# Optimization experiments

Measured on AMD Instinct MI355X. Metric: run time of the kernel, lower is better.

Reference implementation:

```python
import jax, jax.numpy as jnp
import numpy as np

# ---- static config (matches init_kwargs) ----
WS = 7            # window_size
SHIFT = 3         # shift_size (SW-MSA block)
Z, X, Y = 14, 28, 56
DIM = 384
HEADS = 12
HD = DIM // HEADS
N = WS ** 3       # tokens per 3D window = 343
SCALE = HD ** (-0.5)
TBL = (2 * WS - 1) ** 3
B = 2
L = Z * X * Y
NW = (Z // WS) * (X // WS) * (Y // WS)  # 64 windows
MLP_H = 4 * DIM


def _rel_index():
    # Faithful to source: only coords 0 and 1 are offset, coord 0 scaled by (2*Wx-1).
    c = np.stack(np.meshgrid(np.arange(WS), np.arange(WS), np.arange(WS), indexing='ij')).reshape(3, -1)
    r = (c[:, :, None] - c[:, None, :]).transpose(1, 2, 0).astype(np.int64)
    r[..., 0] += WS - 1
    r[..., 1] += WS - 1
    r[..., 0] *= 2 * WS - 1
    idx = r.sum(-1)
    return np.mod(idx, TBL)  # torch wraps negative indices; mod reproduces that

REL_IDX = jnp.asarray(_rel_index())  # (N, N)


def _attn_mask():
    img = np.zeros((1, Z, X, Y, 1))
    sl = (slice(0, -WS), slice(-WS, -SHIFT), slice(-SHIFT, None))
    cnt = 0
    for a in sl:
        for b in sl:
            for c in sl:
                img[:, a, b, c, :] = cnt
                cnt += 1
    w = img.reshape(1, Z // WS, WS, X // WS, WS, Y // WS, WS, 1)
    w = w.transpose(0, 1, 3, 5, 2, 4, 6, 7).reshape(-1, N)
    d = w[:, None, :] - w[:, :, None]
    return np.where(d != 0, -100.0, 0.0).astype(np.float32)  # (NW, N, N)

ATTN_MASK = jnp.asarray(_attn_mask())


def _ln(x, g, b):
    m = x.mean(-1, keepdims=True)
    v = jnp.mean(jnp.square(x - m), axis=-1, keepdims=True)
    return (x - m) * jax.lax.rsqrt(v + 1e-5) * g + b


def _window_partition(x):  # (B,Z,X,Y,C) -> (B*NW, N, C)
    x = x.reshape(B, Z // WS, WS, X // WS, WS, Y // WS, WS, DIM)
    x = x.transpose(0, 1, 3, 5, 2, 4, 6, 7)
    return x.reshape(-1, N, DIM)


def _window_reverse(w):  # (B*NW, N, C) -> (B,Z,X,Y,C)
    x = w.reshape(B, Z // WS, X // WS, Y // WS, WS, WS, WS, DIM)
    x = x.transpose(0, 1, 4, 2, 5, 3, 6, 7)
    return x.reshape(B, Z, X, Y, DIM)


def setup_inputs() -> dict:
    key = jax.random.key(0)
    ks = jax.random.split(key, 8)
    f32 = jnp.float32
    p = {}
    p['x'] = jax.random.normal(ks[0], (B, L, DIM), f32)
    p['norm1_g'] = jnp.ones((DIM,), f32)
    p['norm1_b'] = jnp.zeros((DIM,), f32)
    p['qkv_w'] = (jax.random.normal(ks[1], (DIM, 3 * DIM), f32) * 0.02)
    p['qkv_b'] = jnp.zeros((3 * DIM,), f32)
    p['proj_w'] = (jax.random.normal(ks[2], (DIM, DIM), f32) * 0.02)
    p['proj_b'] = jnp.zeros((DIM,), f32)
    p['rel_tbl'] = (jax.random.normal(ks[3], (TBL, HEADS), f32) * 0.02)
    p['norm2_g'] = jnp.ones((DIM,), f32)
    p['norm2_b'] = jnp.zeros((DIM,), f32)
    p['fc1_w'] = (jax.random.normal(ks[4], (DIM, MLP_H), f32) * 0.02)
    p['fc1_b'] = jnp.zeros((MLP_H,), f32)
    p['fc2_w'] = (jax.random.normal(ks[5], (MLP_H, DIM), f32) * 0.02)
    p['fc2_b'] = jnp.zeros((DIM,), f32)
    return p


def reference(x, norm1_g, norm1_b, qkv_w, qkv_b, proj_w, proj_b, rel_tbl,
              norm2_g, norm2_b, fc1_w, fc1_b, fc2_w, fc2_b):
    shortcut = x
    h = _ln(x, norm1_g, norm1_b).reshape(B, Z, X, Y, DIM)
    # cyclic shift
    h = jnp.roll(h, (-SHIFT, -SHIFT, -SHIFT), axis=(1, 2, 3))
    w = _window_partition(h)                       # (B*NW, N, C)
    qkv = (w @ qkv_w + qkv_b).reshape(-1, N, 3, HEADS, HD).transpose(2, 0, 3, 1, 4)
    q, k, v = qkv[0] * SCALE, qkv[1], qkv[2]       # (B*NW, H, N, hd)
    attn = jnp.einsum('bhnd,bhmd->bhnm', q, k)
    bias = rel_tbl[REL_IDX].transpose(2, 0, 1)     # (H, N, N)
    attn = attn + bias[None]
    attn = attn.reshape(B, NW, HEADS, N, N) + ATTN_MASK[None, :, None]
    attn = jax.nn.softmax(attn.reshape(-1, HEADS, N, N), axis=-1)
    o = jnp.einsum('bhnm,bhmd->bhnd', attn, v).transpose(0, 2, 1, 3).reshape(-1, N, DIM)
    o = o @ proj_w + proj_b
    h = _window_reverse(o)
    h = jnp.roll(h, (SHIFT, SHIFT, SHIFT), axis=(1, 2, 3)).reshape(B, L, DIM)
    x = shortcut + h
    m = _ln(x, norm2_g, norm2_b)
    m = jax.nn.gelu(m @ fc1_w + fc1_b, approximate=False) @ fc2_w + fc2_b
    return x + m
```

## Files before the change

### kernel.cpp

```cpp
#include <hip/hip_runtime.h>
#include <hip/hip_bf16.h>
#include <cmath>

typedef float f32x4 __attribute__((ext_vector_type(4)));
typedef float f32x16 __attribute__((ext_vector_type(16)));
typedef short bf16x8 __attribute__((ext_vector_type(8)));
typedef const __attribute__((address_space(1))) unsigned int* gas_t;
typedef __attribute__((address_space(3))) unsigned int* las_t;

#define GLOAD16(g, l) __builtin_amdgcn_global_load_lds((gas_t)(const void*)(g), (las_t)(void*)(l), 16, 0, 0)

#define LOG2E 1.4426950408889634f
#define MASKC (-144.2695040888963f)
#define SL2E  (0.17677669529663687f * 1.4426950408889634f)

static __device__ __forceinline__ float bf2f(unsigned short u){
  return __uint_as_float(((unsigned)u) << 16);
}
static __device__ __forceinline__ unsigned short f2bf(float f){
  unsigned u = __float_as_uint(f);
  unsigned r = u + 0x7FFFu + ((u >> 16) & 1u);
  return (unsigned short)(r >> 16);
}
static __device__ __forceinline__ unsigned packbf(float a, float b){
  union { __hip_bfloat162 h; unsigned u; } cv;
  cv.h = __float22bfloat162_rn(make_float2(a, b));
  return cv.u;
}
static __device__ __forceinline__ f32x16 zero16(){
  f32x16 z;
  #pragma unroll
  for (int i = 0; i < 16; i++) z[i] = 0.f;
  return z;
}

__global__ __launch_bounds__(256) void padzero_kernel(unsigned short* __restrict__ qs2,
                                                      unsigned short* __restrict__ ks2,
                                                      unsigned short* __restrict__ vt2){
  const int wh = blockIdx.x;
  uint4 z = make_uint4(0, 0, 0, 0);
  const size_t base = (size_t)wh * 11264 + 10 * 1024;
  for (int i = threadIdx.x; i < 384; i += 256){
    int arr = i >> 7, slot = i & 127;
    unsigned short* p = (arr == 0 ? qs2 : (arr == 1 ? ks2 : vt2));
    *(uint4*)(p + base + slot * 8) = z;
  }
}

__global__ __launch_bounds__(256) void wconv2_kernel(const float* __restrict__ in,
                                                     unsigned short* __restrict__ out,
                                                     int K, int N){
  __shared__ unsigned short t[32][33];
  int tx = threadIdx.x & 31, ty = threadIdx.x >> 5;
  int n0 = blockIdx.x * 32, k0 = blockIdx.y * 32;
  #pragma unroll
  for (int i = 0; i < 4; i++)
    t[ty + 8 * i][tx] = f2bf(in[(size_t)(k0 + ty + 8 * i) * N + n0 + tx]);
  __syncthreads();
  #pragma unroll
  for (int i = 0; i < 4; i++)
    out[(size_t)(n0 + ty + 8 * i) * K + k0 + tx] = t[tx][ty + 8 * i];
}

__global__ void biasprep_kernel(const float* __restrict__ rel, unsigned short* __restrict__ bias12){
  int p = blockIdx.x * 256 + threadIdx.x;
  if (p >= 743424) return;
  int h = p / 61952;
  int rem = p - h * 61952;
  int q = rem / 176;
  int m2 = (rem - q * 176) * 2;
  int qi0 = q / 49, qr = q - qi0 * 49, qi1 = qr / 7, qi2 = qr - qi1 * 7;
  unsigned v[2];
  #pragma unroll
  for (int j = 0; j < 2; j++){
    int m = m2 + j;
    float val;
    if (m >= 343) val = -1.4426950e30f;
    else {
      int mi0 = m / 49, mr = m - mi0 * 49, mi1 = mr / 7, mi2 = mr - mi1 * 7;
      int idx = 13 * (qi0 - mi0 + 6) + (qi1 - mi1 + 6) + (qi2 - mi2);
      if (idx < 0) idx += 2197;
      val = rel[idx * 12 + h] * LOG2E;
    }
    v[j] = f2bf(val);
  }
  *(unsigned*)(&bias12[(size_t)h * 123904 + q * 352 + m2]) = v[0] | (v[1] << 16);
}

__global__ void maskprep_kernel(unsigned* __restrict__ bitmapG){
  int id = blockIdx.x * 256 + threadIdx.x;
  if (id >= 8 * 352) return;
  int cls = id / 352, q = id - cls * 352;
  int qi0 = q / 49, qr = q - qi0 * 49, qi1 = qr / 7, qi2 = qr - qi1 * 7;
  int az = (cls & 4) ? (qi0 < 4 ? 1 : 2) : 0;
  int ax = (cls & 2) ? (qi1 < 4 ? 1 : 2) : 0;
  int ay = (cls & 1) ? (qi2 < 4 ? 1 : 2) : 0;
  int cq = az * 9 + ax * 3 + ay;
  unsigned w[11];
  #pragma unroll
  for (int t = 0; t < 11; t++) w[t] = 0u;
  for (int m = 0; m < 352; m++){
    int mi0 = m / 49, mr = m - mi0 * 49, mi1 = mr / 7, mi2 = mr - mi1 * 7;
    int bz = (cls & 4) ? (mi0 < 4 ? 1 : 2) : 0;
    int bx = (cls & 2) ? (mi1 < 4 ? 1 : 2) : 0;
    int by = (cls & 1) ? (mi2 < 4 ? 1 : 2) : 0;
    if (bz * 9 + bx * 3 + by != cq) w[m >> 5] |= (1u << (m & 31));
  }
  unsigned* dst = bitmapG + (size_t)id * 12;
  #pragma unroll
  for (int t = 0; t < 11; t++) dst[t] = w[t];
  dst[11] = 0u;
}

template<int MODE>
__global__ __launch_bounds__(256) void ln_kernel(const float* __restrict__ in,
                                                 const float* __restrict__ g,
                                                 const float* __restrict__ bta,
                                                 unsigned short* __restrict__ out){
  int wave = threadIdx.x >> 6, lane = threadIdx.x & 63;
  int row = blockIdx.x * 4 + wave;
  size_t srow;
  if (MODE == 0){
    int win = row / 343, n = row - win * 343;
    int b = win >> 6, w64 = win & 63;
    int zw = w64 >> 5, xw = (w64 >> 3) & 3, yw = w64 & 7;
    int i0 = n / 49, nr = n - i0 * 49, i1 = nr / 7, i2 = nr - i1 * 7;
    int zs = zw * 7 + i0 + 3; if (zs >= 14) zs -= 14;
    int xs = xw * 7 + i1 + 3; if (xs >= 28) xs -= 28;
    int ys = yw * 7 + i2 + 3; if (ys >= 56) ys -= 56;
    srow = (size_t)b * 21952 + zs * 1568 + xs * 56 + ys;
  } else {
    srow = (size_t)row;
  }
  const float* p = in + srow * 384;
  float v[6]; float s = 0.f;
  #pragma unroll
  for (int i = 0; i < 6; i++){ v[i] = p[lane + i * 64]; s += v[i]; }
  #pragma unroll
  for (int off = 32; off >= 1; off >>= 1) s += __shfl_xor(s, off);
  float mean = s * (1.f / 384.f);
  float vs = 0.f;
  #pragma unroll
  for (int i = 0; i < 6; i++){ float d = v[i] - mean; vs += d * d; }
  #pragma unroll
  for (int off = 32; off >= 1; off >>= 1) vs += __shfl_xor(vs, off);
  float rstd = rsqrtf(vs * (1.f / 384.f) + 1e-5f);
  unsigned short* o = out + (size_t)row * 384;
  #pragma unroll
  for (int i = 0; i < 6; i++){
    int c = lane + i * 64;
    o[c] = f2bf((v[i] - mean) * rstd * g[c] + bta[c]);
  }
}

template<int EPI>
__global__ __launch_bounds__(256, 4) void gemm2(
    const unsigned short* __restrict__ A,
    const unsigned short* __restrict__ Bt,
    const float* __restrict__ bias,
    const float* __restrict__ resid,
    void* __restrict__ outp,
    unsigned short* __restrict__ oq,
    unsigned short* __restrict__ ok,
    unsigned short* __restrict__ ov,
    int K, int ldc, int nt_){
  __shared__ unsigned short Smem[8192];
  unsigned short* As = Smem;
  unsigned short* Bs = Smem + 4096;
  const int nwg = gridDim.x;
  const int qq = nwg >> 3, rr = nwg & 7;
  const int xcd = blockIdx.x & 7, pos = blockIdx.x >> 3;
  const int wgid = (xcd < rr ? xcd * (qq + 1) : rr * (qq + 1) + (xcd - rr) * qq) + pos;
  const int mtile = wgid / nt_, ntile = wgid - mtile * nt_;
  const int r0 = mtile * 128, c0 = ntile * 128;

  const int tid = threadIdx.x, lane = tid & 63, wave = tid >> 6;
  const int wr = (wave >> 1) * 64, wc = (wave & 1) * 64;
  f32x4 acc[4][4];
  #pragma unroll
  for (int mi = 0; mi < 4; mi++)
    #pragma unroll
    for (int ni = 0; ni < 4; ni++) acc[mi][ni] = f32x4{0.f, 0.f, 0.f, 0.f};

  const int srow = lane >> 2;
  const int koff = ((lane & 3) ^ ((lane >> 3) & 3)) * 8;
  const int kkey = (lane >> 1) & 3;

  for (int k0 = 0; k0 < K; k0 += 32){
    __syncthreads();
    #pragma unroll
    for (int i = 0; i < 4; i++){
      int id = wave + i * 4;
      int arr = id >> 3, sub = id & 7;
      const unsigned short* g = (arr ? Bt : A)
          + (size_t)((arr ? c0 : r0) + sub * 16 + srow) * K + k0 + koff;
      unsigned short* dst = (arr ? Bs : As) + sub * 512;
      GLOAD16(g, dst);
    }
    __syncthreads();
    bf16x8 af[4], bfr[4];
    #pragma unroll
    for (int mi = 0; mi < 4; mi++)
      af[mi] = *(const bf16x8*)(&As[(wr + mi * 16 + (lane & 15)) * 32 + (((lane >> 4) ^ kkey) * 8)]);
    #pragma unroll
    for (int ni = 0; ni < 4; ni++)
      bfr[ni] = *(const bf16x8*)(&Bs[(wc + ni * 16 + (lane & 15)) * 32 + (((lane >> 4) ^ kkey) * 8)]);
    #pragma unroll
    for (int mi = 0; mi < 4; mi++)
      #pragma unroll
      for (int ni = 0; ni < 4; ni++)
        acc[mi][ni] = __builtin_amdgcn_mfma_f32_16x16x32_bf16(af[mi], bfr[ni], acc[mi][ni], 0, 0, 0);
  }

  __syncthreads();
  float* ep = (float*)Smem + wave * 1024;
  const int lr = lane & 15;
  const int kx0 = (lr & 7) ^ ((lr >> 2) & 2);
  #pragma unroll
  for (int mi = 0; mi < 4; mi++){
    #pragma unroll
    for (int ni = 0; ni < 4; ni++){
      #pragma unroll
      for (int j = 0; j < 4; j++){
        const int wrow = (lane >> 4) * 4 + j;
        const int col  = ni * 16 + (lane & 15);
        const int key  = ((wrow & 7) << 3) ^ ((wrow & 8) << 1);
        float val = acc[mi][ni][j] + bias[c0 + wc + col];
        if (EPI == 2){
          val = val / (1.0f + exp2f(val * -2.4554669f));
        } else if (EPI == 0){
          if (c0 < 384) val *= SL2E;
        }
        ep[wrow * 64 + (col ^ key)] = val;
      }
    }
    asm volatile("s_waitcnt lgkmcnt(0)" ::: "memory");
    #pragma unroll
    for (int rep = 0; rep < 2; rep++){
      const int cg = (lane >> 4) + rep * 4;
      const float* src = ep + lr * 64 + ((cg ^ kx0) << 3);
      f32x4 v0 = *(const f32x4*)(src);
      f32x4 v1 = *(const f32x4*)(src + 4);
      const int row  = r0 + wr + mi * 16 + lr;
      const int colg = c0 + wc + cg * 8;
      if (EPI == 2){
        uint4 st;
        st.x = packbf(v0[0], v0[1]); st.y = packbf(v0[2], v0[3]);
        st.z = packbf(v1[0], v1[1]); st.w = packbf(v1[2], v1[3]);
        *(uint4*)((unsigned short*)outp + (size_t)row * ldc + colg) = st;
      } else if (EPI == 3){
        const float* rsd = resid + (size_t)row * ldc + colg;
        f32x4 q0 = *(const f32x4*)rsd, q1 = *(const f32x4*)(rsd + 4);
        v0 += q0; v1 += q1;
        float* dst = (float*)outp + (size_t)row * ldc + colg;
        *(f32x4*)dst = v0; *(f32x4*)(dst + 4) = v1;
      } else if (EPI == 1){
        const int win = row / 343, m = row - win * 343;
        const int b = win >> 6, w64 = win & 63;
        const int zw = w64 >> 5, xw = (w64 >> 3) & 3, yw = w64 & 7;
        const int i0 = m / 49, nr = m - i0 * 49, i1 = nr / 7, i2 = nr - i1 * 7;
        int zf = zw * 7 + i0 + 3; if (zf >= 14) zf -= 14;
        int xf = xw * 7 + i1 + 3; if (xf >= 28) xf -= 28;
        int yf = yw * 7 + i2 + 3; if (yf >= 56) yf -= 56;
        const size_t dst = ((size_t)b * 21952 + zf * 1568 + xf * 56 + yf) * 384 + colg;
        const float* rsd = resid + dst;
        f32x4 q0 = *(const f32x4*)rsd, q1 = *(const f32x4*)(rsd + 4);
        v0 += q0; v1 += q1;
        float* dp = (float*)outp + dst;
        *(f32x4*)dp = v0; *(f32x4*)(dp + 4) = v1;
      } else {
        const int win = row / 343, m = row - win * 343;
        const int t = m >> 5, mloc = m & 31;
        if (c0 < 768){
          const int d = (c0 < 384) ? colg : (colg - 384);
          const int h = d >> 5, dd = d & 31;
          unsigned short* basep = (c0 < 384) ? oq : ok;
          const size_t off = (size_t)(win * 12 + h) * 11264
              + (size_t)(t * 1024 + ((dd >> 4) & 1) * 512 + ((dd >> 3) & 1) * 256 + mloc * 8);
          uint4 st;
          st.x = packbf(v0[0], v0[1]); st.y = packbf(v0[2], v0[3]);
          st.z = packbf(v1[0], v1[1]); st.w = packbf(v1[2], v1[3]);
          *(uint4*)(basep + off) = st;
        } else {
          const int d = colg - 768;
          const int h = d >> 5, ddb = d & 31;
          const int vh2 = ((m >> 4) & 1) * 512 + ((m >> 3) & 1) * 256 + (m & 7);
          const size_t off = (size_t)(win * 12 + h) * 11264 + (size_t)(t * 1024 + vh2);
          float vv[8];
          vv[0] = v0[0]; vv[1] = v0[1]; vv[2] = v0[2]; vv[3] = v0[3];
          vv[4] = v1[0]; vv[5] = v1[1]; vv[6] = v1[2]; vv[7] = v1[3];
          #pragma unroll
          for (int jj = 0; jj < 8; jj++)
            ov[off + (size_t)(ddb + jj) * 8] = f2bf(vv[jj]);
        }
      }
    }
    asm volatile("s_waitcnt lgkmcnt(0)" ::: "memory");
  }
}

__global__ __launch_bounds__(256, 4) void attn3_kernel(
    const unsigned short* __restrict__ qs2,
    const unsigned short* __restrict__ ks2,
    const unsigned short* __restrict__ vt2,
    const unsigned short* __restrict__ bias12,
    const unsigned* __restrict__ bitmapG,
    unsigned short* __restrict__ out){
  __shared__ unsigned short Ks[11264];
  __shared__ unsigned short Ps[4][1280];
  const int wh = blockIdx.x;
  const int win = wh / 12, h = wh - win * 12;
  const int tid = threadIdx.x, wave = tid >> 6, lane = tid & 63;
  const int ln = lane & 31, hh = lane >> 5;

  const unsigned short* ksrc = ks2 + (size_t)wh * 11264;
  for (int c = wave; c < 22; c += 4)
    GLOAD16(ksrc + c * 512 + lane * 8, &Ks[c * 512]);

  const int w64 = win & 63;
  const int cls = ((((w64 >> 5) & 1) == 1 ? 4 : 0)) | ((((w64 >> 3) & 3) == 3) ? 2 : 0) | (((w64 & 7) == 7) ? 1 : 0);
  __syncthreads();

  const unsigned short* qbase = qs2 + (size_t)wh * 11264;
  const unsigned short* vbase = vt2 + (size_t)wh * 11264;

  for (int qt = wave; qt < 11; qt += 4){
    const int q_lane = qt * 32 + ln;
    const bf16x8 bq0 = *(const bf16x8*)(qbase + qt * 1024 + hh * 256 + ln * 8);
    const bf16x8 bq1 = *(const bf16x8*)(qbase + qt * 1024 + 512 + hh * 256 + ln * 8);
    const unsigned short* brow = bias12 + ((size_t)h * 352 + q_lane) * 352;
    const unsigned* mrow = bitmapG + (size_t)(cls * 352 + q_lane) * 12;

    f32x16 o = zero16();
    float sum = 0.f;
    bf16x8 nbv0 = *(const bf16x8*)(vbase + hh * 256 + ln * 8);
    bf16x8 nbv1 = *(const bf16x8*)(vbase + 512 + hh * 256 + ln * 8);
    ushort4 nb0 = *(const ushort4*)(brow + hh * 4);
    ushort4 nb1 = *(const ushort4*)(brow + 8 + hh * 4);
    ushort4 nb2 = *(const ushort4*)(brow + 16 + hh * 4);
    ushort4 nb3 = *(const ushort4*)(brow + 24 + hh * 4);
    unsigned nwm = mrow[0];

    for (int t = 0; t < 11; t++){
      const bf16x8 bv0 = nbv0, bv1 = nbv1;
      const ushort4 cb0 = nb0, cb1 = nb1, cb2 = nb2, cb3 = nb3;
      const unsigned wm = nwm;
      if (t < 10){
        const unsigned short* vnext = vbase + (t + 1) * 1024;
        nbv0 = *(const bf16x8*)(vnext + hh * 256 + ln * 8);
        nbv1 = *(const bf16x8*)(vnext + 512 + hh * 256 + ln * 8);
        const unsigned short* bnext = brow + (t + 1) * 32;
        nb0 = *(const ushort4*)(bnext + hh * 4);
        nb1 = *(const ushort4*)(bnext + 8 + hh * 4);
        nb2 = *(const ushort4*)(bnext + 16 + hh * 4);
        nb3 = *(const ushort4*)(bnext + 24 + hh * 4);
        nwm = mrow[t + 1];
      }
      const bf16x8 ka0 = *(const bf16x8*)(&Ks[t * 1024 + hh * 256 + ln * 8]);
      const bf16x8 ka1 = *(const bf16x8*)(&Ks[t * 1024 + 512 + hh * 256 + ln * 8]);
      f32x16 acc = zero16();
      acc = __builtin_amdgcn_mfma_f32_32x32x16_bf16(ka0, bq0, acc, 0, 0, 0);
      acc = __builtin_amdgcn_mfma_f32_32x32x16_bf16(ka1, bq1, acc, 0, 0, 0);

      const unsigned wsh = wm >> (4 * hh);
      float pv[16];
      unsigned short cbv[16];
      *(ushort4*)(&cbv[0]) = cb0; *(ushort4*)(&cbv[4]) = cb1;
      *(ushort4*)(&cbv[8]) = cb2; *(ushort4*)(&cbv[12]) = cb3;
      #pragma unroll
      for (int g = 0; g < 4; g++){
        #pragma unroll
        for (int i = 0; i < 4; i++){
          const int r = g * 4 + i;
          float s = acc[r] + bf2f(cbv[r]);
          if (cls){
            if (wsh & (1u << (i + 8 * g))) s += MASKC;
          }
          float e = exp2f(s);
          sum += e;
          pv[r] = e;
        }
      }
      #pragma unroll
      for (int g = 0; g < 4; g++){
        uint2 pk;
        pk.x = packbf(pv[4 * g], pv[4 * g + 1]);
        pk.y = packbf(pv[4 * g + 2], pv[4 * g + 3]);
        *(uint2*)(&Ps[wave][ln * 40 + 8 * g + 4 * hh]) = pk;
      }
      const bf16x8 pa0 = *(const bf16x8*)(&Ps[wave][ln * 40 + 8 * hh]);
      const bf16x8 pa1 = *(const bf16x8*)(&Ps[wave][ln * 40 + 16 + 8 * hh]);
      o = __builtin_amdgcn_mfma_f32_32x32x16_bf16(pa0, bv0, o, 0, 0, 0);
      o = __builtin_amdgcn_mfma_f32_32x32x16_bf16(pa1, bv1, o, 0, 0, 0);
    }
    sum += __shfl_xor(sum, 32);
    const float inv = 1.f / sum;
    #pragma unroll
    for (int r = 0; r < 16; r++){
      const int qloc = (r & 3) + 8 * (r >> 2) + 4 * hh;
      const float iv = __shfl(inv, qloc);
      const int qg = qt * 32 + qloc;
      if (qg < 343)
        out[((size_t)win * 343 + qg) * 384 + h * 32 + ln] = f2bf(o[r] * iv);
    }
  }
}

extern "C" void kernel_launch(void* const* d_in, const int* in_sizes, int n_in,
                              void* d_out, int out_size, void* d_ws, size_t ws_size,
                              hipStream_t stream){
  const float* x      = (const float*)d_in[0];
  const float* n1g    = (const float*)d_in[1];
  const float* n1b    = (const float*)d_in[2];
  const float* qkv_w  = (const float*)d_in[3];
  const float* qkv_b  = (const float*)d_in[4];
  const float* proj_w = (const float*)d_in[5];
  const float* proj_b = (const float*)d_in[6];
  const float* rel    = (const float*)d_in[7];
  const float* n2g    = (const float*)d_in[8];
  const float* n2b    = (const float*)d_in[9];
  const float* fc1_w  = (const float*)d_in[10];
  const float* fc1_b  = (const float*)d_in[11];
  const float* fc2_w  = (const float*)d_in[12];
  const float* fc2_b  = (const float*)d_in[13];
  float* out = (float*)d_out;

  char* ws = (char*)d_ws;
  unsigned short* w_win  = (unsigned short*)(ws + 0);
  unsigned short* hidden = (unsigned short*)(ws + 0);
  unsigned short* qs2    = (unsigned short*)(ws + 33718272ull);
  unsigned short* ks2    = (unsigned short*)(ws + 68321280ull);
  unsigned short* vt2    = (unsigned short*)(ws + 102924288ull);
  float*          x2     = (float*)(ws + 134873088ull);
  unsigned short* bias12 = (unsigned short*)(ws + 137527296ull);
  unsigned*       bitmapG= (unsigned*)(ws + 140504064ull);
  unsigned short* att    = (unsigned short*)(ws + 202309632ull);
  unsigned short* ln2    = att;
  unsigned short* wt_qkv = (unsigned short*)(ws + 236027904ull);
  unsigned short* wt_prj = (unsigned short*)(ws + 236912640ull);
  unsigned short* wt_fc1 = (unsigned short*)(ws + 237207552ull);
  unsigned short* wt_fc2 = (unsigned short*)(ws + 238387200ull);

  wconv2_kernel<<<dim3(36, 12), 256, 0, stream>>>(qkv_w, wt_qkv, 384, 1152);
  wconv2_kernel<<<dim3(12, 12), 256, 0, stream>>>(proj_w, wt_prj, 384, 384);
  wconv2_kernel<<<dim3(48, 12), 256, 0, stream>>>(fc1_w, wt_fc1, 384, 1536);
  wconv2_kernel<<<dim3(12, 48), 256, 0, stream>>>(fc2_w, wt_fc2, 1536, 384);
  biasprep_kernel<<<2904, 256, 0, stream>>>(rel, bias12);
  maskprep_kernel<<<11, 256, 0, stream>>>(bitmapG);
  padzero_kernel<<<1536, 256, 0, stream>>>(qs2, ks2, vt2);

  ln_kernel<0><<<10976, 256, 0, stream>>>(x, n1g, n1b, w_win);
  gemm2<0><<<343 * 9, 256, 0, stream>>>(w_win, wt_qkv, qkv_b, nullptr, nullptr,
                                        qs2, ks2, vt2, 384, 0, 9);
  attn3_kernel<<<1536, 256, 0, stream>>>(qs2, ks2, vt2, bias12, bitmapG, att);
  gemm2<1><<<343 * 3, 256, 0, stream>>>(att, wt_prj, proj_b, x, x2,
                                        nullptr, nullptr, nullptr, 384, 384, 3);
  ln_kernel<1><<<10976, 256, 0, stream>>>(x2, n2g, n2b, ln2);
  gemm2<2><<<343 * 12, 256, 0, stream>>>(ln2, wt_fc1, fc1_b, nullptr, hidden,
                                         nullptr, nullptr, nullptr, 384, 1536, 12);
  gemm2<3><<<343 * 3, 256, 0, stream>>>(hidden, wt_fc2, fc2_b, x2, out,
                                        nullptr, nullptr, nullptr, 1536, 384, 3);
}
```

Measured before the change: 526.3 us.

## Double-buffer per-wave GEMM tiles with async LDS loads and drop block barriers

Result: slower. 592.8 us (+12.6%).

```diff
diff --git a/kernel.cpp b/kernel.cpp
--- a/kernel.cpp
+++ b/kernel.cpp
@@ -154,7 +154,7 @@
 }
 
 template<int EPI>
-__global__ __launch_bounds__(256, 4) void gemm2(
+__global__ __launch_bounds__(256, 2) void gemm2(
     const unsigned short* __restrict__ A,
     const unsigned short* __restrict__ Bt,
     const float* __restrict__ bias,
@@ -164,9 +164,7 @@
     unsigned short* __restrict__ ok,
     unsigned short* __restrict__ ov,
     int K, int ldc, int nt_){
-  __shared__ unsigned short Smem[8192];
-  unsigned short* As = Smem;
-  unsigned short* Bs = Smem + 4096;
+  __shared__ unsigned short W[4][2][2][2048];
   const int nwg = gridDim.x;
   const int qq = nwg >> 3, rr = nwg & 7;
   const int xcd = blockIdx.x & 7, pos = blockIdx.x >> 3;
@@ -185,37 +183,53 @@
   const int srow = lane >> 2;
   const int koff = ((lane & 3) ^ ((lane >> 3) & 3)) * 8;
   const int kkey = (lane >> 1) & 3;
-
-  for (int k0 = 0; k0 < K; k0 += 32){
-    __syncthreads();
-    #pragma unroll
-    for (int i = 0; i < 4; i++){
-      int id = wave + i * 4;
-      int arr = id >> 3, sub = id & 7;
-      const unsigned short* g = (arr ? Bt : A)
-          + (size_t)((arr ? c0 : r0) + sub * 16 + srow) * K + k0 + koff;
-      unsigned short* dst = (arr ? Bs : As) + sub * 512;
-      GLOAD16(g, dst);
-    }
-    __syncthreads();
+  const int nt = K >> 5;
+
+  #define STAGE(T) do {                                                        \
+    const int b_ = (T) & 1;                                                    \
+    const int k0_ = (T) << 5;                                                  \
+    _Pragma("unroll")                                                          \
+    for (int i_ = 0; i_ < 4; i_++){                                            \
+      const unsigned short* ga_ = A + (size_t)(r0 + wr + i_ * 16 + srow) * K + k0_ + koff; \
+      GLOAD16(ga_, &W[wave][b_][0][i_ * 512]);                                 \
+    }                                                                          \
+    _Pragma("unroll")                                                          \
+    for (int i_ = 0; i_ < 4; i_++){                                            \
+      const unsigned short* gb_ = Bt + (size_t)(c0 + wc + i_ * 16 + srow) * K + k0_ + koff; \
+      GLOAD16(gb_, &W[wave][b_][1][i_ * 512]);                                 \
+    }                                                                          \
+  } while (0)
+
+  STAGE(0);
+  STAGE(1);
+  for (int t = 0; t < nt; t++){
+    if (t < nt - 1) asm volatile("s_waitcnt vmcnt(8)" ::: "memory");
+    else            asm volatile("s_waitcnt vmcnt(0)" ::: "memory");
+    const int b = t & 1;
     bf16x8 af[4], bfr[4];
     #pragma unroll
     for (int mi = 0; mi < 4; mi++)
-      af[mi] = *(const bf16x8*)(&As[(wr + mi * 16 + (lane & 15)) * 32 + (((lane >> 4) ^ kkey) * 8)]);
+      af[mi] = *(const bf16x8*)(&W[wave][b][0][(mi * 16 + (lane & 15)) * 32 + (((lane >> 4) ^ kkey) * 8)]);
     #pragma unroll
     for (int ni = 0; ni < 4; ni++)
-      bfr[ni] = *(const bf16x8*)(&Bs[(wc + ni * 16 + (lane & 15)) * 32 + (((lane >> 4) ^ kkey) * 8)]);
+      bfr[ni] = *(const bf16x8*)(&W[wave][b][1][(ni * 16 + (lane & 15)) * 32 + (((lane >> 4) ^ kkey) * 8)]);
+    asm volatile("s_waitcnt lgkmcnt(0)" ::: "memory");
+    if (t + 2 < nt) STAGE(t + 2);
+    __builtin_amdgcn_sched_barrier(0);
+    __builtin_amdgcn_s_setprio(1);
     #pragma unroll
     for (int mi = 0; mi < 4; mi++)
       #pragma unroll
       for (int ni = 0; ni < 4; ni++)
         acc[mi][ni] = __builtin_amdgcn_mfma_f32_16x16x32_bf16(af[mi], bfr[ni], acc[mi][ni], 0, 0, 0);
-  }
-
-  __syncthreads();
-  float* ep = (float*)Smem + wave * 1024;
+    __builtin_amdgcn_s_setprio(0);
+  }
+  #undef STAGE
+
+  asm volatile("s_waitcnt lgkmcnt(0)" ::: "memory");
+  float* ep = (float*)&W[wave][0][0][0];
   const int lr = lane & 15;
-  const int kx0 = (lr & 7) ^ ((lr >> 2) & 2);
+  const int kx0 = (lr & 7) ^ ((lr & 12) >> 1);
   #pragma unroll
   for (int mi = 0; mi < 4; mi++){
     #pragma unroll
@@ -224,7 +238,7 @@
       for (int j = 0; j < 4; j++){
         const int wrow = (lane >> 4) * 4 + j;
         const int col  = ni * 16 + (lane & 15);
-        const int key  = ((wrow & 7) << 3) ^ ((wrow & 8) << 1);
+        const int key  = ((wrow & 7) << 3) ^ ((wrow & 12) << 2);
         float val = acc[mi][ni][j] + bias[c0 + wc + col];
         if (EPI == 2){
           val = val / (1.0f + exp2f(val * -2.4554669f));
@@ -238,7 +252,7 @@
     #pragma unroll
     for (int rep = 0; rep < 2; rep++){
       const int cg = (lane >> 4) + rep * 4;
-      const float* src = ep + lr * 64 + ((cg ^ kx0) << 3);
+      const float* src = ep + lr * 64 + (((cg ^ kx0) & 7) << 3);
       f32x4 v0 = *(const f32x4*)(src);
       f32x4 v1 = *(const f32x4*)(src + 4);
       const int row  = r0 + wr + mi * 16 + lr;
```
